# Optimization experiments

Hardware: AMD Instinct MI355X
Metric: run time of the kernel (lower is better)

The kernel has to match this reference:

```python
import jax, jax.numpy as jnp
import numpy as np

B, N, H, W = 64, 32, 200, 200


def setup_inputs() -> dict:
    key = jax.random.key(0)
    k1, k2, k3, k4 = jax.random.split(key, 4)
    return {
        "parameter": jax.random.uniform(k1, (B, N, 3), dtype=jnp.float32),
        "x_start": jax.random.uniform(k2, (), dtype=jnp.float32),
        "y_start": jax.random.uniform(k3, (), dtype=jnp.float32),
        "theta": jax.random.uniform(k4, (), dtype=jnp.float32, minval=-3.14159, maxval=3.14159),
        # learned parameters at their torch init values
        "weights": jnp.eye(2, dtype=jnp.float32),
        "biases": jnp.zeros(2, dtype=jnp.float32),
        "thick_mult": jnp.array(0.5, dtype=jnp.float32),
        "thick_bias": jnp.array(0.1, dtype=jnp.float32),
        "dark_exp": jnp.array(1.0, dtype=jnp.float32),
        "dark_non_lin_weight": jnp.array(0.5, dtype=jnp.float32),
        "x_m": jnp.array(1.0, dtype=jnp.float32),
        "y_m": jnp.array(1.0, dtype=jnp.float32),
        "x_b": jnp.array(0.0, dtype=jnp.float32),
        "y_b": jnp.array(0.0, dtype=jnp.float32),
        "use_conv": 0,
    }


def reference(parameter, x_start, y_start, theta, weights, biases, thick_mult,
              thick_bias, dark_exp, dark_non_lin_weight, x_m, y_m, x_b, y_b,
              use_conv):
    # torch.flip(traj, dims=(2,)) then traj[:,:,0] *= -1:
    # channel0 (y) = -parameter[...,1], channel1 (x) = parameter[...,0]
    y0 = -parameter[..., 1]
    x0 = parameter[..., 0]
    # rotation about origin (vectorized over batch; identical per-element math)
    c, s = jnp.cos(theta), jnp.sin(theta)
    x_rot = x0 * c + y0 * s
    y_rot = -x0 * s + y0 * c
    yy = y_rot * y_m + y_b + y_start
    xx = x_rot * x_m + x_b + x_start
    traj = jnp.stack([yy, xx], axis=-1)                      # (B,N,2)
    # curve_to_stroke: matmul(weights, curve).T + biases == traj @ weights.T + biases
    strokes = traj @ weights.T + biases                      # (B,N,2)
    thick = (parameter[..., 2] * 2.0 + 0.5) / 64.0           # (B,N)
    # grid_coords: channel0 = row/H, channel1 = col/W
    gy = jnp.arange(H, dtype=strokes.dtype) / H
    gx = jnp.arange(W, dtype=strokes.dtype) / W
    coords = jnp.stack(jnp.meshgrid(gy, gx, indexing='ij'), axis=-1)  # (H,W,2)
    v = strokes[:, :-1, None, None, :]                       # (B,N-1,1,1,2)
    w = strokes[:, 1:, None, None, :]
    p = coords[None, None]                                   # (1,1,H,W,2)
    wv = w - v
    d2 = jnp.sum(wv * wv, axis=-1)                           # (B,N-1,1,1)
    dot = jnp.sum((p - v) * wv, axis=-1) / (d2 + 1e-5)       # (B,N-1,H,W)
    frac = jnp.clip(dot, 0.0, 1.0)
    proj = v + frac[..., None] * wv                          # (B,N-1,H,W,2)
    diff = p - proj
    dist = jnp.sqrt(jnp.sum(diff * diff, axis=-1))           # (B,N-1,H,W)
    th = thick[:, :-1, None, None] * (1.0 - frac) + thick[:, 1:, None, None] * frac
    th = jnp.maximum(th * thick_mult + thick_bias, 1e-8)
    dark = jnp.clip((th - dist) / th, 0.0, 1.0)
    dark = (dark + 1e-4) ** dark_exp
    nl = jax.nn.sigmoid(dark * 16.0 - 8.0)
    dark = dark_non_lin_weight * nl + (1.0 - dark_non_lin_weight) * dark
    return jnp.max(dark, axis=1)                             # (B,H,W)
```

## Files before the change

### kernel.cpp

```cpp
#include <hip/hip_runtime.h>
#include <math.h>

#define B_ 64
#define N_ 32
#define H_ 200
#define W_ 200
#define NSEG (N_ - 1)
#define TS 16
#define NT 13
#define TILE_RAD 0.056f

__global__ __launch_bounds__(256) void stroke_kernel(
    const float* __restrict__ param,
    const float* __restrict__ x_start,
    const float* __restrict__ y_start,
    const float* __restrict__ theta,
    const float* __restrict__ weights,
    const float* __restrict__ biases,
    const float* __restrict__ thick_mult,
    const float* __restrict__ thick_bias,
    const float* __restrict__ dark_exp_p,
    const float* __restrict__ dark_nlw_p,
    const float* __restrict__ x_m_p,
    const float* __restrict__ y_m_p,
    const float* __restrict__ x_b_p,
    const float* __restrict__ y_b_p,
    float* __restrict__ out)
{
    __shared__ float4 s_A[NSEG];
    __shared__ float4 s_B[NSEG];
    __shared__ float s_sy[N_], s_sx[N_], s_tk[N_];
    __shared__ int s_cnt;

    const int b   = blockIdx.z;
    const int tid = threadIdx.x;

    const float thv  = theta[0];
    const float c    = cosf(thv), s = sinf(thv);
    const float xs   = x_start[0], ys = y_start[0];
    const float W00  = weights[0], W01 = weights[1];
    const float W10  = weights[2], W11 = weights[3];
    const float bb0  = biases[0],  bb1 = biases[1];
    const float tm   = thick_mult[0], tb = thick_bias[0];
    const float dexp = dark_exp_p[0], dnlw = dark_nlw_p[0];
    const float xm   = x_m_p[0], ym = y_m_p[0];
    const float xb   = x_b_p[0], yb = y_b_p[0];

    if (tid < N_) {
        float p0 = param[(b * N_ + tid) * 3 + 0];
        float p1 = param[(b * N_ + tid) * 3 + 1];
        float p2 = param[(b * N_ + tid) * 3 + 2];
        float x0 = p0, y0 = -p1;
        float x_rot =  x0 * c + y0 * s;
        float y_rot = -x0 * s + y0 * c;
        float yy = y_rot * ym + yb + ys;
        float xx = x_rot * xm + xb + xs;
        s_sy[tid] = yy * W00 + xx * W01 + bb0;
        s_sx[tid] = yy * W10 + xx * W11 + bb1;
        s_tk[tid] = (p2 * 2.0f + 0.5f) * (1.0f / 64.0f);
    }
    __syncthreads();

    const float cy = ((float)(blockIdx.y * TS) + 7.5f) * (1.0f / H_);
    const float cx = ((float)(blockIdx.x * TS) + 7.5f) * (1.0f / W_);

    bool keep = false;
    float4 A4, B4;
    if (tid < NSEG) {
        float vy = s_sy[tid],     vx = s_sx[tid];
        float wy = s_sy[tid + 1], wx = s_sx[tid + 1];
        float wvy = wy - vy, wvx = wx - vx;
        float d2 = wvy * wvy + wvx * wvx;
        float inv_d2 = 1.0f / (d2 + 1e-5f);
        float t0 = s_tk[tid], t1 = s_tk[tid + 1];
        float c0 = t0 * tm + tb;
        float c1 = (t1 - t0) * tm;
        A4 = make_float4(vy, vx, wvy, wvx);
        B4 = make_float4(inv_d2, c0, c1, 0.0f);
        float dyc = cy - vy, dxc = cx - vx;
        float dot = (dyc * wvy + dxc * wvx) * inv_d2;
        float fr  = fminf(fmaxf(dot, 0.0f), 1.0f);
        float ey  = dyc - fr * wvy;
        float ex  = dxc - fr * wvx;
        float e2c = ey * ey + ex * ex;
        float thmax = fmaxf(fmaxf(c0, c0 + c1), 1e-8f);
        float reach = thmax + TILE_RAD;
        keep = e2c < reach * reach;
    }
    if (tid < 64) {
        unsigned long long mask = __ballot(keep);
        int pos = (int)__popcll(mask & ((1ull << tid) - 1ull));
        if (keep) { s_A[pos] = A4; s_B[pos] = B4; }
        if (tid == 0) s_cnt = (int)__popcll(mask);
    }
    __syncthreads();

    const int cnt = s_cnt;
    const int ii = tid >> 4, jj = tid & 15;
    const int i = blockIdx.y * TS + ii;
    const int j = blockIdx.x * TS + jj;
    const float py = (float)i * (1.0f / H_);
    const float px = (float)j * (1.0f / W_);

    const bool hoist = (dexp > 0.0f) && (dnlw >= 0.0f) && (dnlw <= 1.0f);

    float result;
    if (hoist) {
        float qmin = INFINITY;
        if (cnt > 0) {
            float4 A = s_A[0], Bc = s_B[0];
            for (int n = 0; n < cnt; ++n) {
                int np = (n + 1 < cnt) ? n + 1 : n;
                float4 An = s_A[np], Bn = s_B[np];
                float dy  = py - A.x;
                float dx  = px - A.y;
                float dot = fmaf(dy, A.z, dx * A.w) * Bc.x;
                float fr  = fminf(fmaxf(dot, 0.0f), 1.0f);
                float ey  = fmaf(-fr, A.z, dy);
                float ex  = fmaf(-fr, A.w, dx);
                float e2  = fmaf(ey, ey, ex * ex);
                float th  = fmaxf(fmaf(fr, Bc.z, Bc.y), 1e-8f);
                float ith = __builtin_amdgcn_rcpf(th);
                float q   = (e2 * ith) * ith;
                qmin = fminf(qmin, q);
                A = An; Bc = Bn;
            }
        }
        float md = fminf(fmaxf(1.0f - __builtin_amdgcn_sqrtf(qmin), 0.0f), 1.0f);
        float d  = __expf(dexp * __logf(md + 1e-4f));
        float nl = __builtin_amdgcn_rcpf(1.0f + __expf(8.0f - d * 16.0f));
        result = dnlw * nl + (1.0f - dnlw) * d;
    } else {
        float best = -INFINITY;
        if (cnt < NSEG) {
            float d0  = __expf(dexp * __logf(1e-4f));
            float nl0 = __builtin_amdgcn_rcpf(1.0f + __expf(8.0f - d0 * 16.0f));
            best = dnlw * nl0 + (1.0f - dnlw) * d0;
        }
        for (int n = 0; n < cnt; ++n) {
            float4 A = s_A[n], Bc = s_B[n];
            float dy  = py - A.x;
            float dx  = px - A.y;
            float dot = fmaf(dy, A.z, dx * A.w) * Bc.x;
            float fr  = fminf(fmaxf(dot, 0.0f), 1.0f);
            float ey  = fmaf(-fr, A.z, dy);
            float ex  = fmaf(-fr, A.w, dx);
            float e2  = fmaf(ey, ey, ex * ex);
            float dist = __builtin_amdgcn_sqrtf(e2);
            float th  = fmaxf(fmaf(fr, Bc.z, Bc.y), 1e-8f);
            float dark = fminf(fmaxf(fmaf(-dist, __builtin_amdgcn_rcpf(th), 1.0f), 0.0f), 1.0f);
            float d  = __expf(dexp * __logf(dark + 1e-4f));
            float nl = __builtin_amdgcn_rcpf(1.0f + __expf(8.0f - d * 16.0f));
            best = fmaxf(best, dnlw * nl + (1.0f - dnlw) * d);
        }
        result = best;
    }

    if (i < H_ && j < W_)
        out[(b * H_ + i) * W_ + j] = result;
}

extern "C" void kernel_launch(void* const* d_in, const int* in_sizes, int n_in,
                              void* d_out, int out_size, void* d_ws, size_t ws_size,
                              hipStream_t stream) {
    const float* param      = (const float*)d_in[0];
    const float* x_start    = (const float*)d_in[1];
    const float* y_start    = (const float*)d_in[2];
    const float* theta      = (const float*)d_in[3];
    const float* weights    = (const float*)d_in[4];
    const float* biases     = (const float*)d_in[5];
    const float* thick_mult = (const float*)d_in[6];
    const float* thick_bias = (const float*)d_in[7];
    const float* dark_exp   = (const float*)d_in[8];
    const float* dark_nlw   = (const float*)d_in[9];
    const float* x_m        = (const float*)d_in[10];
    const float* y_m        = (const float*)d_in[11];
    const float* x_b        = (const float*)d_in[12];
    const float* y_b        = (const float*)d_in[13];
    float* out = (float*)d_out;

    dim3 block(256);
    dim3 grid(NT, NT, B_);
    stroke_kernel<<<grid, block, 0, stream>>>(
        param, x_start, y_start, theta, weights, biases,
        thick_mult, thick_bias, dark_exp, dark_nlw,
        x_m, y_m, x_b, y_b, out);
}
```

Baseline: 16.21 us.

## Compute two horizontal pixels per thread and build segments with wave shuffles

Each thread now computes two adjacent pixels, using a 32x16 tile and a float2 store. Per segment it reuses the segment loads, dy, and the dot product, getting the second pixel's projection with a precomputed increment. Segment setup now runs in a single wavefront using shuffles instead of shared memory, which removes one barrier. The larger tile needs a bigger culling radius, so more segments pass the cull for each block, and the grid has fewer blocks.

```diff
diff --git a/kernel.cpp b/kernel.cpp
--- a/kernel.cpp
+++ b/kernel.cpp
@@ -6,9 +6,11 @@
 #define H_ 200
 #define W_ 200
 #define NSEG (N_ - 1)
-#define TS 16
-#define NT 13
-#define TILE_RAD 0.056f
+#define TSX 32
+#define TSY 16
+#define NTX 7
+#define NTY 13
+#define TILE_RAD 0.087f
 
 __global__ __launch_bounds__(256) void stroke_kernel(
     const float* __restrict__ param,
@@ -29,65 +31,63 @@
 {
     __shared__ float4 s_A[NSEG];
     __shared__ float4 s_B[NSEG];
-    __shared__ float s_sy[N_], s_sx[N_], s_tk[N_];
     __shared__ int s_cnt;
 
     const int b   = blockIdx.z;
     const int tid = threadIdx.x;
 
-    const float thv  = theta[0];
-    const float c    = cosf(thv), s = sinf(thv);
-    const float xs   = x_start[0], ys = y_start[0];
-    const float W00  = weights[0], W01 = weights[1];
-    const float W10  = weights[2], W11 = weights[3];
-    const float bb0  = biases[0],  bb1 = biases[1];
-    const float tm   = thick_mult[0], tb = thick_bias[0];
     const float dexp = dark_exp_p[0], dnlw = dark_nlw_p[0];
-    const float xm   = x_m_p[0], ym = y_m_p[0];
-    const float xb   = x_b_p[0], yb = y_b_p[0];
-
-    if (tid < N_) {
-        float p0 = param[(b * N_ + tid) * 3 + 0];
-        float p1 = param[(b * N_ + tid) * 3 + 1];
-        float p2 = param[(b * N_ + tid) * 3 + 2];
-        float x0 = p0, y0 = -p1;
-        float x_rot =  x0 * c + y0 * s;
-        float y_rot = -x0 * s + y0 * c;
-        float yy = y_rot * ym + yb + ys;
-        float xx = x_rot * xm + xb + xs;
-        s_sy[tid] = yy * W00 + xx * W01 + bb0;
-        s_sx[tid] = yy * W10 + xx * W11 + bb1;
-        s_tk[tid] = (p2 * 2.0f + 0.5f) * (1.0f / 64.0f);
-    }
-    __syncthreads();
-
-    const float cy = ((float)(blockIdx.y * TS) + 7.5f) * (1.0f / H_);
-    const float cx = ((float)(blockIdx.x * TS) + 7.5f) * (1.0f / W_);
-
-    bool keep = false;
-    float4 A4, B4;
-    if (tid < NSEG) {
-        float vy = s_sy[tid],     vx = s_sx[tid];
-        float wy = s_sy[tid + 1], wx = s_sx[tid + 1];
-        float wvy = wy - vy, wvx = wx - vx;
-        float d2 = wvy * wvy + wvx * wvx;
-        float inv_d2 = 1.0f / (d2 + 1e-5f);
-        float t0 = s_tk[tid], t1 = s_tk[tid + 1];
-        float c0 = t0 * tm + tb;
-        float c1 = (t1 - t0) * tm;
-        A4 = make_float4(vy, vx, wvy, wvx);
-        B4 = make_float4(inv_d2, c0, c1, 0.0f);
-        float dyc = cy - vy, dxc = cx - vx;
-        float dot = (dyc * wvy + dxc * wvx) * inv_d2;
-        float fr  = fminf(fmaxf(dot, 0.0f), 1.0f);
-        float ey  = dyc - fr * wvy;
-        float ex  = dxc - fr * wvx;
-        float e2c = ey * ey + ex * ex;
-        float thmax = fmaxf(fmaxf(c0, c0 + c1), 1e-8f);
-        float reach = thmax + TILE_RAD;
-        keep = e2c < reach * reach;
-    }
+
     if (tid < 64) {
+        float sy = 0.0f, sx = 0.0f, tk = 0.0f;
+        const float tm = thick_mult[0], tb = thick_bias[0];
+        if (tid < N_) {
+            const float thv = theta[0];
+            const float c   = cosf(thv), s = sinf(thv);
+            const float xs  = x_start[0], ys = y_start[0];
+            const float W00 = weights[0], W01 = weights[1];
+            const float W10 = weights[2], W11 = weights[3];
+            const float bb0 = biases[0],  bb1 = biases[1];
+            const float xm  = x_m_p[0], ym = y_m_p[0];
+            const float xb  = x_b_p[0], yb = y_b_p[0];
+            float p0 = param[(b * N_ + tid) * 3 + 0];
+            float p1 = param[(b * N_ + tid) * 3 + 1];
+            float p2 = param[(b * N_ + tid) * 3 + 2];
+            float x0 = p0, y0 = -p1;
+            float x_rot =  x0 * c + y0 * s;
+            float y_rot = -x0 * s + y0 * c;
+            float yy = y_rot * ym + yb + ys;
+            float xx = x_rot * xm + xb + xs;
+            sy = yy * W00 + xx * W01 + bb0;
+            sx = yy * W10 + xx * W11 + bb1;
+            tk = (p2 * 2.0f + 0.5f) * (1.0f / 64.0f);
+        }
+        float sy1 = __shfl_down(sy, 1);
+        float sx1 = __shfl_down(sx, 1);
+        float tk1 = __shfl_down(tk, 1);
+
+        bool keep = false;
+        float4 A4 = make_float4(0,0,0,0), B4 = make_float4(0,0,0,0);
+        if (tid < NSEG) {
+            float wvy = sy1 - sy, wvx = sx1 - sx;
+            float d2 = wvy * wvy + wvx * wvx;
+            float inv_d2 = 1.0f / (d2 + 1e-5f);
+            float c0 = tk * tm + tb;
+            float c1 = (tk1 - tk) * tm;
+            A4 = make_float4(sy, sx, wvy, wvx);
+            B4 = make_float4(inv_d2, c0, c1, wvx * inv_d2 * (1.0f / W_));
+            const float cy = ((float)(blockIdx.y * TSY) + 7.5f)  * (1.0f / H_);
+            const float cx = ((float)(blockIdx.x * TSX) + 15.5f) * (1.0f / W_);
+            float dyc = cy - sy, dxc = cx - sx;
+            float dot = (dyc * wvy + dxc * wvx) * inv_d2;
+            float fr  = fminf(fmaxf(dot, 0.0f), 1.0f);
+            float ey  = dyc - fr * wvy;
+            float ex  = dxc - fr * wvx;
+            float e2c = ey * ey + ex * ex;
+            float thmax = fmaxf(fmaxf(c0, c0 + c1), 1e-8f);
+            float reach = thmax + TILE_RAD;
+            keep = e2c < reach * reach;
+        }
         unsigned long long mask = __ballot(keep);
         int pos = (int)__popcll(mask & ((1ull << tid) - 1ull));
         if (keep) { s_A[pos] = A4; s_B[pos] = B4; }
@@ -97,67 +97,100 @@
 
     const int cnt = s_cnt;
     const int ii = tid >> 4, jj = tid & 15;
-    const int i = blockIdx.y * TS + ii;
-    const int j = blockIdx.x * TS + jj;
-    const float py = (float)i * (1.0f / H_);
-    const float px = (float)j * (1.0f / W_);
+    const int i  = blockIdx.y * TSY + ii;
+    const int j0 = blockIdx.x * TSX + (jj << 1);
+    const float py  = (float)i  * (1.0f / H_);
+    const float px0 = (float)j0 * (1.0f / W_);
+    const float px1 = px0 + (1.0f / W_);
 
     const bool hoist = (dexp > 0.0f) && (dnlw >= 0.0f) && (dnlw <= 1.0f);
 
-    float result;
+    float r0, r1;
     if (hoist) {
-        float qmin = INFINITY;
+        float q0m = INFINITY, q1m = INFINITY;
         if (cnt > 0) {
             float4 A = s_A[0], Bc = s_B[0];
             for (int n = 0; n < cnt; ++n) {
                 int np = (n + 1 < cnt) ? n + 1 : n;
                 float4 An = s_A[np], Bn = s_B[np];
-                float dy  = py - A.x;
-                float dx  = px - A.y;
-                float dot = fmaf(dy, A.z, dx * A.w) * Bc.x;
-                float fr  = fminf(fmaxf(dot, 0.0f), 1.0f);
-                float ey  = fmaf(-fr, A.z, dy);
-                float ex  = fmaf(-fr, A.w, dx);
-                float e2  = fmaf(ey, ey, ex * ex);
-                float th  = fmaxf(fmaf(fr, Bc.z, Bc.y), 1e-8f);
-                float ith = __builtin_amdgcn_rcpf(th);
-                float q   = (e2 * ith) * ith;
-                qmin = fminf(qmin, q);
+                float dy  = py  - A.x;
+                float dx0 = px0 - A.y;
+                float dx1 = px1 - A.y;
+                float dot0 = fmaf(dy, A.z, dx0 * A.w) * Bc.x;
+                float dot1 = dot0 + Bc.w;
+                float fr0 = __builtin_amdgcn_fmed3f(dot0, 0.0f, 1.0f);
+                float fr1 = __builtin_amdgcn_fmed3f(dot1, 0.0f, 1.0f);
+                float ey0 = fmaf(-fr0, A.z, dy);
+                float ex0 = fmaf(-fr0, A.w, dx0);
+                float e20 = fmaf(ey0, ey0, ex0 * ex0);
+                float th0 = fmaxf(fmaf(fr0, Bc.z, Bc.y), 1e-8f);
+                float it0 = __builtin_amdgcn_rcpf(th0);
+                q0m = fminf(q0m, (e20 * it0) * it0);
+                float ey1 = fmaf(-fr1, A.z, dy);
+                float ex1 = fmaf(-fr1, A.w, dx1);
+                float e21 = fmaf(ey1, ey1, ex1 * ex1);
+                float th1 = fmaxf(fmaf(fr1, Bc.z, Bc.y), 1e-8f);
+                float it1 = __builtin_amdgcn_rcpf(th1);
+                q1m = fminf(q1m, (e21 * it1) * it1);
                 A = An; Bc = Bn;
             }
         }
-        float md = fminf(fmaxf(1.0f - __builtin_amdgcn_sqrtf(qmin), 0.0f), 1.0f);
-        float d  = __expf(dexp * __logf(md + 1e-4f));
-        float nl = __builtin_amdgcn_rcpf(1.0f + __expf(8.0f - d * 16.0f));
-        result = dnlw * nl + (1.0f - dnlw) * d;
+        {
+            float md = fminf(fmaxf(1.0f - __builtin_amdgcn_sqrtf(q0m), 0.0f), 1.0f);
+            float d  = __expf(dexp * __logf(md + 1e-4f));
+            float nl = __builtin_amdgcn_rcpf(1.0f + __expf(8.0f - d * 16.0f));
+            r0 = dnlw * nl + (1.0f - dnlw) * d;
+        }
+        {
+            float md = fminf(fmaxf(1.0f - __builtin_amdgcn_sqrtf(q1m), 0.0f), 1.0f);
+            float d  = __expf(dexp * __logf(md + 1e-4f));
+            float nl = __builtin_amdgcn_rcpf(1.0f + __expf(8.0f - d * 16.0f));
+            r1 = dnlw * nl + (1.0f - dnlw) * d;
+        }
     } else {
-        float best = -INFINITY;
+        float b0 = -INFINITY, b1 = -INFINITY;
         if (cnt < NSEG) {
             float d0  = __expf(dexp * __logf(1e-4f));
             float nl0 = __builtin_amdgcn_rcpf(1.0f + __expf(8.0f - d0 * 16.0f));
-            best = dnlw * nl0 + (1.0f - dnlw) * d0;
+            float t0  = dnlw * nl0 + (1.0f - dnlw) * d0;
+            b0 = t0; b1 = t0;
         }
         for (int n = 0; n < cnt; ++n) {
             float4 A = s_A[n], Bc = s_B[n];
-            float dy  = py - A.x;
-            float dx  = px - A.y;
-            float dot = fmaf(dy, A.z, dx * A.w) * Bc.x;
-            float fr  = fminf(fmaxf(dot, 0.0f), 1.0f);
-            float ey  = fmaf(-fr, A.z, dy);
-            float ex  = fmaf(-fr, A.w, dx);
-            float e2  = fmaf(ey, ey, ex * ex);
-            float dist = __builtin_amdgcn_sqrtf(e2);
-            float th  = fmaxf(fmaf(fr, Bc.z, Bc.y), 1e-8f);
-            float dark = fminf(fmaxf(fmaf(-dist, __builtin_amdgcn_rcpf(th), 1.0f), 0.0f), 1.0f);
-            float d  = __expf(dexp * __logf(dark + 1e-4f));
-            float nl = __builtin_amdgcn_rcpf(1.0f + __expf(8.0f - d * 16.0f));
-            best = fmaxf(best, dnlw * nl + (1.0f - dnlw) * d);
-        }
-        result = best;
+            float dy  = py  - A.x;
+            float dx0 = px0 - A.y;
+            float dx1 = px1 - A.y;
+            float dot0 = fmaf(dy, A.z, dx0 * A.w) * Bc.x;
+            float dot1 = dot0 + Bc.w;
+            float fr0 = __builtin_amdgcn_fmed3f(dot0, 0.0f, 1.0f);
+            float fr1 = __builtin_amdgcn_fmed3f(dot1, 0.0f, 1.0f);
+            {
+                float ey = fmaf(-fr0, A.z, dy);
+                float ex = fmaf(-fr0, A.w, dx0);
+                float dist = __builtin_amdgcn_sqrtf(fmaf(ey, ey, ex * ex));
+                float th = fmaxf(fmaf(fr0, Bc.z, Bc.y), 1e-8f);
+                float dark = fminf(fmaxf(fmaf(-dist, __builtin_amdgcn_rcpf(th), 1.0f), 0.0f), 1.0f);
+                float d  = __expf(dexp * __logf(dark + 1e-4f));
+                float nl = __builtin_amdgcn_rcpf(1.0f + __expf(8.0f - d * 16.0f));
+                b0 = fmaxf(b0, dnlw * nl + (1.0f - dnlw) * d);
+            }
+            {
+                float ey = fmaf(-fr1, A.z, dy);
+                float ex = fmaf(-fr1, A.w, dx1);
+                float dist = __builtin_amdgcn_sqrtf(fmaf(ey, ey, ex * ex));
+                float th = fmaxf(fmaf(fr1, Bc.z, Bc.y), 1e-8f);
+                float dark = fminf(fmaxf(fmaf(-dist, __builtin_amdgcn_rcpf(th), 1.0f), 0.0f), 1.0f);
+                float d  = __expf(dexp * __logf(dark + 1e-4f));
+                float nl = __builtin_amdgcn_rcpf(1.0f + __expf(8.0f - d * 16.0f));
+                b1 = fmaxf(b1, dnlw * nl + (1.0f - dnlw) * d);
+            }
+        }
+        r0 = b0; r1 = b1;
     }
 
-    if (i < H_ && j < W_)
-        out[(b * H_ + i) * W_ + j] = result;
+    if (i < H_ && j0 < W_) {
+        *reinterpret_cast<float2*>(&out[(b * H_ + i) * W_ + j0]) = make_float2(r0, r1);
+    }
 }
 
 extern "C" void kernel_launch(void* const* d_in, const int* in_sizes, int n_in,
@@ -180,7 +213,7 @@
     float* out = (float*)d_out;
 
     dim3 block(256);
-    dim3 grid(NT, NT, B_);
+    dim3 grid(NTX, NTY, B_);
     stroke_kernel<<<grid, block, 0, stream>>>(
         param, x_start, y_start, theta, weights, biases,
         thick_mult, thick_bias, dark_exp, dark_nlw,
```

Result: faster. 14.37 us (-11.4%).
